# Kernel tuning notes

Measured on AMD Instinct MI355X. Metric: run time of the kernel, lower is better.

The kernel has to match this reference:

```python
import jax, jax.numpy as jnp
import numpy as np

NUM_ENTITIES = 100000
NUM_TIMES = 10000
D = 512
DB = 768
NUM_REL = 200
NUM_BASES = 4
N_NODES = 30000
N_EDGES = 200000
B = 128
P_ENT = 64
P_TIME = 32
T_UNIQ = 2000


def setup_inputs() -> dict:
    key = jax.random.key(0)
    ks = jax.random.split(key, 32)
    n = jax.random.normal
    ri = jax.random.randint
    inp = {}
    # learned params
    inp['emb'] = n(ks[0], (NUM_ENTITIES + NUM_TIMES, D), jnp.float32) * 0.05
    sc = 1.0 / np.sqrt(D)
    inp['basis1'] = n(ks[1], (NUM_BASES, D, D), jnp.float32) * sc
    inp['att1'] = n(ks[2], (NUM_REL, NUM_BASES), jnp.float32) * 0.5
    inp['root1'] = n(ks[3], (D, D), jnp.float32) * sc
    inp['bias1'] = jnp.zeros((D,), jnp.float32)
    inp['basis2'] = n(ks[4], (NUM_BASES, D, D), jnp.float32) * sc
    inp['att2'] = n(ks[5], (NUM_REL, NUM_BASES), jnp.float32) * 0.5
    inp['root2'] = n(ks[6], (D, D), jnp.float32) * sc
    inp['bias2'] = jnp.zeros((D,), jnp.float32)
    sb = 1.0 / np.sqrt(DB)
    inp['W_lin'] = n(ks[7], (DB, D), jnp.float32) * sb
    inp['b_lin'] = jnp.zeros((D,), jnp.float32)
    inp['W_attn'] = n(ks[8], (DB, D), jnp.float32) * sb
    inp['b_attn'] = jnp.zeros((D,), jnp.float32)
    inp['W_prob'] = n(ks[9], (DB, 1), jnp.float32) * sb
    inp['b_prob'] = jnp.zeros((1,), jnp.float32)
    # forward tensor args
    inp['ques_emb_bert'] = n(ks[10], (B, DB), jnp.float32)
    inp['x_idx'] = ri(ks[11], (N_NODES,), 0, NUM_ENTITIES, jnp.int32)
    inp['edge_index'] = ri(ks[12], (2, N_EDGES), 0, N_NODES, jnp.int32)
    inp['edge_type'] = ri(ks[13], (N_EDGES,), 0, NUM_REL, jnp.int32)
    inp['start_time'] = ri(ks[14], (N_EDGES,), 0, NUM_TIMES, jnp.int32)
    inp['end_time'] = ri(ks[15], (N_EDGES,), 0, NUM_TIMES, jnp.int32)
    inp['edge_batch_idx'] = jnp.sort(ri(ks[16], (N_EDGES,), 0, B, jnp.int32))
    inp['edge_norm'] = jax.random.uniform(ks[17], (N_EDGES,), jnp.float32)
    inp['uniq_times'] = ri(ks[18], (T_UNIQ,), 0, NUM_TIMES, jnp.int32)
    # padded index vectors: positions >= count point at the appended zero row
    ent_counts = ri(ks[19], (B,), 1, P_ENT + 1, jnp.int32)
    time_counts = ri(ks[20], (B,), 1, P_TIME + 1, jnp.int32)
    pe = ri(ks[21], (B, P_ENT), 0, N_NODES, jnp.int32)
    pt = ri(ks[22], (B, P_TIME), 0, T_UNIQ, jnp.int32)
    inp['padded_ent'] = jnp.where(jnp.arange(P_ENT)[None, :] < ent_counts[:, None], pe, N_NODES)
    inp['padded_time'] = jnp.where(jnp.arange(P_TIME)[None, :] < time_counts[:, None], pt, T_UNIQ)
    inp['ent_counts'] = ent_counts
    inp['time_counts'] = time_counts
    return inp


def rgcn_layer(x, basis, att, root, bias, src, dst, etype, st_emb, et_emb, q_t, edge_norm):
    # basis decomposition: project all nodes through each basis once. [N, NB, D]
    xb = jnp.einsum('ni,bio->nbo', x, basis)
    coeff = att[etype]                                 # [E, NB]
    msg = jnp.einsum('eb,ebd->ed', coeff, xb[src])     # [E, D]
    # time gate: question-time embedding vs edge interval midpoint embedding
    gate = jax.nn.sigmoid(jnp.sum(q_t * 0.5 * (st_emb + et_emb), axis=-1))  # [E]
    msg = msg * (gate * edge_norm)[:, None]
    agg = jax.ops.segment_sum(msg, dst, num_segments=N_NODES)
    return agg + x @ root + bias


def reference(emb, basis1, att1, root1, bias1, basis2, att2, root2, bias2,
              W_lin, b_lin, W_attn, b_attn, W_prob, b_prob,
              ques_emb_bert, x_idx, edge_index, edge_type, start_time, end_time,
              edge_batch_idx, edge_norm, uniq_times, padded_ent, padded_time,
              ent_counts, time_counts):
    question_embedding = ques_emb_bert @ W_lin + b_lin                  # [B, D]
    time_for_edge_attn = (ques_emb_bert @ W_attn + b_attn)[edge_batch_idx]  # [E, D]
    st_emb = emb[start_time + NUM_ENTITIES]
    et_emb = emb[end_time + NUM_ENTITIES]
    x = emb[x_idx]                                                      # [N, D]
    src, dst = edge_index[0], edge_index[1]
    h = jax.nn.relu(rgcn_layer(x, basis1, att1, root1, bias1, src, dst, edge_type,
                               st_emb, et_emb, time_for_edge_attn, edge_norm))
    # dropout is identity in eval mode
    h = rgcn_layer(h, basis2, att2, root2, bias2, src, dst, edge_type,
                   st_emb, et_emb, time_for_edge_attn, edge_norm)       # [N, D]
    subgraph_time_emb = emb[uniq_times + NUM_ENTITIES]                  # [T_u, D]
    zero = jnp.zeros((1, D), h.dtype)
    ent_w_zeros = jnp.concatenate([h, zero], axis=0)
    time_w_zeros = jnp.concatenate([subgraph_time_emb, zero], axis=0)
    pooled_ent = jnp.sum(ent_w_zeros[padded_ent], axis=1) / ent_counts[:, None].astype(h.dtype)
    pooled_time = jnp.sum(time_w_zeros[padded_time], axis=1) / time_counts[:, None].astype(h.dtype)
    p_ent = jax.nn.sigmoid(ques_emb_bert @ W_prob + b_prob)             # [B, 1]
    pred = (question_embedding + pooled_ent * p_ent + pooled_time * (1.0 - p_ent)) / 3.0
    # batched cosine similarity against full entity+time vocab
    pred_n = pred / jnp.maximum(jnp.linalg.norm(pred, axis=-1, keepdims=True), 1e-8)
    emb_n = emb / jnp.maximum(jnp.linalg.norm(emb, axis=-1, keepdims=True), 1e-8)
    score = pred_n @ emb_n.T                                            # [B, V]
    return score * 30.0
```

## Files before the change

kernel.cpp:

```cpp
#include <hip/hip_runtime.h>

#define NUM_ENT   100000
#define NTIMES    10000
#define DD        512
#define DB        768
#define NREL      200
#define NBAS      4
#define NN        30000
#define NEDGE     200000
#define BATCH     128
#define PENT      64
#define PTIME     32
#define TUNIQ     2000
#define V_TOT     110000
#define V_PAD     110208
#define VT16      6888
#define M_PAD2    30208
#define MT2R      1888
#define KT_L      80
#define KT_E      16

typedef __attribute__((ext_vector_type(8))) short s8v;
typedef __attribute__((ext_vector_type(4))) float f4v;

__device__ __forceinline__ unsigned short f2bf(float x){
  unsigned int u = __builtin_bit_cast(unsigned int, x);
  u += 0x7fffu + ((u >> 16) & 1u);
  return (unsigned short)(u >> 16);
}
__device__ __forceinline__ float bf2f(unsigned short h){
  unsigned int u = ((unsigned int)h) << 16;
  return __builtin_bit_cast(float, u);
}

__device__ __forceinline__ void gload16(const void* g, void* l){
  __builtin_amdgcn_global_load_lds(
      (const __attribute__((address_space(1))) void*)g,
      (__attribute__((address_space(3))) void*)l, 16, 0, 0);
}


__global__ __launch_bounds__(256) void k_conv_emb(const float* __restrict__ emb,
    unsigned short* __restrict__ Bp, float* __restrict__ invn){
  int vt = blockIdx.x;
  int wid = threadIdx.x >> 6, lane = threadIdx.x & 63;
  int vrow = vt * 16 + (lane & 15);
  float ss = 0.f;
  __shared__ float ssw[4][16];
  for (int i = 0; i < 4; ++i){
    int kt = wid + i * 4;
    int k0 = kt * 32 + (lane >> 4) * 8;
    s8v o;
    if (vrow < V_TOT){
      const float4* p = reinterpret_cast<const float4*>(emb + (size_t)vrow * DD + k0);
      float4 v0 = p[0], v1 = p[1];
      ss += v0.x*v0.x + v0.y*v0.y + v0.z*v0.z + v0.w*v0.w;
      ss += v1.x*v1.x + v1.y*v1.y + v1.z*v1.z + v1.w*v1.w;
      o[0] = (short)f2bf(v0.x); o[1] = (short)f2bf(v0.y);
      o[2] = (short)f2bf(v0.z); o[3] = (short)f2bf(v0.w);
      o[4] = (short)f2bf(v1.x); o[5] = (short)f2bf(v1.y);
      o[6] = (short)f2bf(v1.z); o[7] = (short)f2bf(v1.w);
    } else {
      #pragma unroll
      for (int j = 0; j < 8; ++j) o[j] = 0;
    }
    *reinterpret_cast<s8v*>(Bp + ((size_t)(kt * VT16 + vt) << 9) + lane * 8) = o;
  }
  ss += __shfl_xor(ss, 16);
  ss += __shfl_xor(ss, 32);
  if ((lane >> 4) == 0) ssw[wid][lane] = ss;
  __syncthreads();
  if (threadIdx.x < 16){
    float s = ssw[0][threadIdx.x] + ssw[1][threadIdx.x] + ssw[2][threadIdx.x] + ssw[3][threadIdx.x];
    int v = vt * 16 + threadIdx.x;
    invn[v] = (v < V_TOT) ? (1.0f / fmaxf(sqrtf(s), 1e-8f)) : 0.0f;
  }
}

__global__ __launch_bounds__(256) void k_small2(const float* __restrict__ ques,
    const float* __restrict__ Wl, const float* __restrict__ bl,
    const float* __restrict__ Wa, const float* __restrict__ ba,
    const float* __restrict__ Wp, const float* __restrict__ bp,
    float* __restrict__ qlin, float* __restrict__ qattn, float* __restrict__ pent){
  if (blockIdx.x == 32){
    int b = threadIdx.x >> 1, half = threadIdx.x & 1;
    float a = 0.f;
    int k0 = half * 384;
    for (int k = k0; k < k0 + 384; ++k)
      a = fmaf(ques[(size_t)b * DB + k], Wp[k], a);
    a += __shfl_xor(a, 1);
    if (half == 0) pent[b] = 1.f / (1.f + expf(-(a + bp[0])));
    return;
  }
  __shared__ float sq[128 * 96];
  int col = threadIdx.x & 31, bg = threadIdx.x >> 5;
  int c0 = blockIdx.x * 32;
  const float* W = (c0 < 512) ? Wl : Wa;
  int wcol = (c0 & 511) + col;
  float acc[16] = {};
  for (int k0 = 0; k0 < DB; k0 += 96){
    __syncthreads();
    for (int i = threadIdx.x; i < 128 * 96; i += 256){
      int b = i / 96, kk = i - b * 96;
      sq[i] = ques[(size_t)b * DB + k0 + kk];
    }
    __syncthreads();
    for (int kk = 0; kk < 96; kk += 4){
      float w0 = W[(size_t)(k0 + kk + 0) * 512 + wcol];
      float w1 = W[(size_t)(k0 + kk + 1) * 512 + wcol];
      float w2 = W[(size_t)(k0 + kk + 2) * 512 + wcol];
      float w3 = W[(size_t)(k0 + kk + 3) * 512 + wcol];
      #pragma unroll
      for (int bb = 0; bb < 16; ++bb){
        float4 qv = *reinterpret_cast<const float4*>(&sq[(bg * 16 + bb) * 96 + kk]);
        acc[bb] = fmaf(qv.x, w0, fmaf(qv.y, w1, fmaf(qv.z, w2, fmaf(qv.w, w3, acc[bb]))));
      }
    }
  }
  float* dst = (c0 < 512) ? qlin : qattn;
  const float* bias = (c0 < 512) ? bl : ba;
  #pragma unroll
  for (int bb = 0; bb < 16; ++bb)
    dst[(size_t)(bg * 16 + bb) * 512 + wcol] = acc[bb] + bias[wcol];
}

__global__ __launch_bounds__(256) void k_pack_qrows(const float* __restrict__ src,
    unsigned short* __restrict__ Ap){
  int w = (int)((blockIdx.x * 256 + threadIdx.x) >> 6);
  int lane = threadIdx.x & 63;
  if (w >= BATCH) return;
  const float* p = src + (size_t)w * 512 + lane * 8;
  s8v o;
  #pragma unroll
  for (int j = 0; j < 8; ++j) o[j] = (short)f2bf(p[j]);
  *reinterpret_cast<s8v*>(Ap + ((size_t)((w >> 4) * KT_E + (lane >> 2)) << 9)
                             + ((w & 15) + (lane & 3) * 16) * 8) = o;
}

__global__ __launch_bounds__(256) void k_pack_B2(
    const float* __restrict__ basis1, const float* __restrict__ root1,
    const float* __restrict__ basis2, const float* __restrict__ root2,
    unsigned short* __restrict__ B1p, unsigned short* __restrict__ B2p){
  int idx = blockIdx.x * 256 + threadIdx.x;
  int set = idx >= KT_L * 32 * 64;
  if (set) idx -= KT_L * 32 * 64;
  const float* basis = set ? basis2 : basis1;
  const float* root  = set ? root2  : root1;
  unsigned short* Bp = set ? B2p : B1p;
  int lane = idx & 63; int kt = idx >> 11;
  int k0 = kt * 32 + (lane >> 4) * 8;
  int col = ((idx >> 6) & 31) * 16 + (lane & 15);
  s8v o;
  #pragma unroll
  for (int j = 0; j < 8; ++j){
    int k = k0 + j;
    float v = (k < 2048) ? basis[(size_t)k * 512 + col] : root[(size_t)(k - 2048) * 512 + col];
    o[j] = (short)f2bf(v);
  }
  *reinterpret_cast<s8v*>(Bp + (size_t)idx * 8) = o;
}

__global__ __launch_bounds__(256) void k_gemm_m2(
    const unsigned short* __restrict__ A, const unsigned short* __restrict__ B,
    float* __restrict__ outf){
  __shared__ __align__(1024) short sAll[3 * 8192];
  const int Kt = KT_E;
  int tid = threadIdx.x;
  int lane = tid & 63, wid = tid >> 6;
  int wr = wid >> 1, wc = wid & 1;
  int rt0 = blockIdx.x * 8;
  int ct0 = blockIdx.y * 8;
  const unsigned short* pA0 = A + ((size_t)(rt0 + 2 * wid) * Kt) * 512 + lane * 8;
  const unsigned short* pA1 = pA0 + (size_t)Kt * 512;
  const unsigned short* pB0 = B + (size_t)(ct0 + 2 * wid) * 512 + lane * 8;
  const unsigned short* pB1 = pB0 + 512;
  size_t gbs = (size_t)VT16 * 512;
  int so = 2 * wid * 512;
  f4v acc[4][4] = {};

  auto STAGE = [&](int buf, int kt){
    short* b = &sAll[buf * 8192];
    gload16(pA0 + (size_t)kt * 512, b + so);
    gload16(pA1 + (size_t)kt * 512, b + so + 512);
    gload16(pB0 + (size_t)kt * gbs, b + 4096 + so);
    gload16(pB1 + (size_t)kt * gbs, b + 4096 + so + 512);
  };
  auto COMPUTE = [&](int buf){
    const short* base = &sAll[buf * 8192];
    s8v af[4], bfr[4];
    #pragma unroll
    for (int m = 0; m < 4; ++m) af[m] = *reinterpret_cast<const s8v*>(base + (wr * 4 + m) * 512 + lane * 8);
    #pragma unroll
    for (int n = 0; n < 4; ++n) bfr[n] = *reinterpret_cast<const s8v*>(base + 4096 + (wc * 4 + n) * 512 + lane * 8);
    #pragma unroll
    for (int m = 0; m < 4; ++m)
      #pragma unroll
      for (int n = 0; n < 4; ++n)
        acc[m][n] = __builtin_amdgcn_mfma_f32_16x16x32_bf16(af[m], bfr[n], acc[m][n], 0, 0, 0);
  };

  STAGE(0, 0);
  STAGE(1, 1);
  int cb = 0, sb = 2;
  for (int kt = 0; kt < Kt - 2; ++kt){
    STAGE(sb, kt + 2);
    asm volatile("s_waitcnt vmcnt(8)" ::: "memory");
    __builtin_amdgcn_s_barrier();
    __builtin_amdgcn_sched_barrier(0);
    COMPUTE(cb);
    __builtin_amdgcn_s_barrier();
    cb = (cb == 2) ? 0 : cb + 1;
    sb = (sb == 2) ? 0 : sb + 1;
  }
  asm volatile("s_waitcnt vmcnt(4)" ::: "memory");
  __builtin_amdgcn_s_barrier();
  __builtin_amdgcn_sched_barrier(0);
  COMPUTE(cb);
  cb = (cb == 2) ? 0 : cb + 1;
  asm volatile("s_waitcnt vmcnt(0)" ::: "memory");
  __builtin_amdgcn_s_barrier();
  __builtin_amdgcn_sched_barrier(0);
  COMPUTE(cb);

  #pragma unroll
  for (int m = 0; m < 4; ++m)
    #pragma unroll
    for (int n = 0; n < 4; ++n){
      int row0 = rt0 * 16 + (wr * 4 + m) * 16 + ((lane >> 4) * 4);
      int col  = (ct0 + wc * 4 + n) * 16 + (lane & 15);
      #pragma unroll
      for (int r = 0; r < 4; ++r){
        int rr = row0 + r;
        if (col < NTIMES) outf[(size_t)rr * NTIMES + col] = acc[m][n][r];
      }
    }
}

__global__ __launch_bounds__(256, 3) void k_score_p(
    const unsigned short* __restrict__ Apred, const unsigned short* __restrict__ Bp,
    const float* __restrict__ invn, float* __restrict__ out){
  __shared__ __align__(1024) short sAll[3 * 8192];
  const int Kt = KT_E;
  int tid = threadIdx.x;
  int lane = tid & 63, wid = tid >> 6;
  int wr = wid >> 1, wc = wid & 1;
  int kq = lane >> 4, r16 = lane & 15;
  int ct0 = blockIdx.x * 8;
  const unsigned short* pA0 = Apred + ((size_t)(2 * wid) * Kt) * 512 + lane * 8;
  const unsigned short* pA1 = pA0 + (size_t)Kt * 512;
  const unsigned short* pB0 = Bp + (size_t)(ct0 + 2 * wid) * 512 + lane * 8;
  const unsigned short* pB1 = pB0 + 512;
  size_t gbs = (size_t)VT16 * 512;
  int so = 2 * wid * 512;
  f4v acc[4][4] = {};

  auto STAGE = [&](int buf, int kt){
    short* b = &sAll[buf * 8192];
    gload16(pA0 + (size_t)kt * 512, b + so);
    gload16(pA1 + (size_t)kt * 512, b + so + 512);
    gload16(pB0 + (size_t)kt * gbs, b + 4096 + so);
    gload16(pB1 + (size_t)kt * gbs, b + 4096 + so + 512);
  };
  auto COMPUTE = [&](int buf){
    const short* base = &sAll[buf * 8192];
    s8v af[4], bfr[4];
    #pragma unroll
    for (int m = 0; m < 4; ++m) af[m] = *reinterpret_cast<const s8v*>(base + (wr * 4 + m) * 512 + lane * 8);
    #pragma unroll
    for (int n = 0; n < 4; ++n) bfr[n] = *reinterpret_cast<const s8v*>(base + 4096 + (wc * 4 + n) * 512 + lane * 8);
    #pragma unroll
    for (int m = 0; m < 4; ++m)
      #pragma unroll
      for (int n = 0; n < 4; ++n)
        acc[m][n] = __builtin_amdgcn_mfma_f32_16x16x32_bf16(af[m], bfr[n], acc[m][n], 0, 0, 0);
  };

  STAGE(0, 0);
  STAGE(1, 1);
  int cb = 0, sb = 2;
  for (int kt = 0; kt < Kt - 2; ++kt){
    STAGE(sb, kt + 2);
    asm volatile("s_waitcnt vmcnt(8)" ::: "memory");
    __builtin_amdgcn_s_barrier();
    __builtin_amdgcn_sched_barrier(0);
    COMPUTE(cb);
    __builtin_amdgcn_s_barrier();
    cb = (cb == 2) ? 0 : cb + 1;
    sb = (sb == 2) ? 0 : sb + 1;
  }
  asm volatile("s_waitcnt vmcnt(4)" ::: "memory");
  __builtin_amdgcn_s_barrier();
  __builtin_amdgcn_sched_barrier(0);
  COMPUTE(cb);
  cb = (cb == 2) ? 0 : cb + 1;
  asm volatile("s_waitcnt vmcnt(0)" ::: "memory");
  __builtin_amdgcn_s_barrier();
  __builtin_amdgcn_sched_barrier(0);
  COMPUTE(cb);

  __syncthreads();
  float* scratch = reinterpret_cast<float*>(sAll) + wid * 2176;
  int colg = ct0 * 16 + wc * 64 + r16 * 4;
  bool c_ok = colg < V_TOT;
  float4 inv4 = float4{0.f, 0.f, 0.f, 0.f};
  if (c_ok){
    inv4 = *reinterpret_cast<const float4*>(invn + colg);
    inv4.x *= 30.f; inv4.y *= 30.f; inv4.z *= 30.f; inv4.w *= 30.f;
  }
  #pragma unroll
  for (int p = 0; p < 2; ++p){
    #pragma unroll
    for (int mm = 0; mm < 2; ++mm){
      int m = p * 2 + mm;
      #pragma unroll
      for (int n = 0; n < 4; ++n)
        #pragma unroll
        for (int r = 0; r < 4; ++r)
          scratch[(mm * 16 + kq * 4 + r) * 68 + n * 16 + r16] = acc[m][n][r];
    }
    #pragma unroll
    for (int i = 0; i < 8; ++i){
      int row_r = i * 4 + kq;
      float4 v = *reinterpret_cast<const float4*>(scratch + row_r * 68 + r16 * 4);
      if (c_ok){
        float4 o;
        o.x = v.x * inv4.x; o.y = v.y * inv4.y; o.z = v.z * inv4.z; o.w = v.w * inv4.w;
        int grr = wr * 64 + p * 32 + row_r;
        *reinterpret_cast<float4*>(out + (size_t)grr * V_TOT + colg) = o;
      }
    }
  }
}

template<int MODE>
__global__ __launch_bounds__(512, 2) void k_gemm512(
    const unsigned short* __restrict__ A, const unsigned short* __restrict__ B,
    const float* __restrict__ bias, unsigned short* __restrict__ outh){
  __shared__ __align__(1024) short sAll[3 * 20480];
  const int Kt = KT_L;
  int tid = threadIdx.x;
  int lane = tid & 63, wid = tid >> 6;
  int wr = wid >> 2, wc = wid & 3;
  int blk = blockIdx.x;
  int rt0 = blk * 8;
  const unsigned short* pA = A + ((size_t)(rt0 + wid) * Kt) * 512 + lane * 8;
  const unsigned short* pB = B + (size_t)(wid * 4) * 512 + lane * 8;
  int soA = wid * 512;
  int soB = 4096 + wid * 4 * 512;
  f4v acc[4][8] = {};

  auto STAGE = [&](int buf, int kt){
    short* b = &sAll[buf * 20480];
    gload16(pA + (size_t)kt * 512, b + soA);
    const unsigned short* pb = pB + (size_t)kt * 32 * 512;
    gload16(pb,        b + soB);
    gload16(pb +  512, b + soB +  512);
    gload16(pb + 1024, b + soB + 1024);
    gload16(pb + 1536, b + soB + 1536);
  };
  auto COMPUTE = [&](int buf){
    const short* base = &sAll[buf * 20480];
    s8v af[4], bfr[8];
    #pragma unroll
    for (int m = 0; m < 4; ++m) af[m] = *reinterpret_cast<const s8v*>(base + (wr * 4 + m) * 512 + lane * 8);
    #pragma unroll
    for (int n = 0; n < 8; ++n) bfr[n] = *reinterpret_cast<const s8v*>(base + 4096 + (wc * 8 + n) * 512 + lane * 8);
    __builtin_amdgcn_s_setprio(1);
    #pragma unroll
    for (int m = 0; m < 4; ++m)
      #pragma unroll
      for (int n = 0; n < 8; ++n)
        acc[m][n] = __builtin_amdgcn_mfma_f32_16x16x32_bf16(af[m], bfr[n], acc[m][n], 0, 0, 0);
    __builtin_amdgcn_s_setprio(0);
  };

  STAGE(0, 0);
  STAGE(1, 1);
  int cb = 0, sb = 2;
  for (int kt = 0; kt < Kt - 2; ++kt){
    STAGE(sb, kt + 2);
    asm volatile("s_waitcnt vmcnt(10)" ::: "memory");
    __builtin_amdgcn_s_barrier();
    __builtin_amdgcn_sched_barrier(0);
    COMPUTE(cb);
    __builtin_amdgcn_s_barrier();
    cb = (cb == 2) ? 0 : cb + 1;
    sb = (sb == 2) ? 0 : sb + 1;
  }
  asm volatile("s_waitcnt vmcnt(5)" ::: "memory");
  __builtin_amdgcn_s_barrier();
  __builtin_amdgcn_sched_barrier(0);
  COMPUTE(cb);
  cb = (cb == 2) ? 0 : cb + 1;
  asm volatile("s_waitcnt vmcnt(0)" ::: "memory");
  __builtin_amdgcn_s_barrier();
  __builtin_amdgcn_sched_barrier(0);
  COMPUTE(cb);

  int R0 = blk * 128 + wr * 64 + ((lane >> 4) * 4);
  int C0 = wc * 128 + (lane & 15);
  #pragma unroll
  for (int m = 0; m < 4; ++m)
    #pragma unroll
    for (int r4 = 0; r4 < 4; ++r4){
      int rr = R0 + m * 16 + r4;
      if (rr < NN){
        #pragma unroll
        for (int n = 0; n < 8; ++n){
          int col = C0 + n * 16;
          float v = acc[m][n][r4] + bias[col];
          if constexpr (MODE == 1) v = fmaxf(v, 0.f);
          outh[(size_t)rr * 512 + col] = f2bf(v);
        }
      }
    }
}

__global__ __launch_bounds__(256) void k_edgeprep(const int* __restrict__ ebatch,
    const int* __restrict__ st, const int* __restrict__ et,
    const float* __restrict__ enorm, const float* __restrict__ M2,
    const int* __restrict__ ei,
    float* __restrict__ we, int* __restrict__ cnt, int* __restrict__ lists){
  int e = blockIdx.x * 256 + threadIdx.x;
  if (e >= NEDGE) return;
  int b = ebatch[e];
  float s = 0.5f * (M2[(size_t)b * NTIMES + st[e]] + M2[(size_t)b * NTIMES + et[e]]);
  we[e] = (1.f / (1.f + expf(-s))) * enorm[e];
  int dst = ei[NEDGE + e];
  int slot = atomicAdd(&cnt[dst], 1);
  if (slot < 64) lists[(size_t)dst * 64 + slot] = e;
}

__global__ __launch_bounds__(256) void k_gather_x(const int* __restrict__ x_idx,
    const float* __restrict__ emb, unsigned short* __restrict__ Ap,
    unsigned short* __restrict__ x_rm){
  int w = (int)((blockIdx.x * 256 + threadIdx.x) >> 6);
  int lane = threadIdx.x & 63;
  if (w >= NN) return;
  int v = x_idx[w];
  const float4* p = reinterpret_cast<const float4*>(emb + (size_t)v * 512 + lane * 8);
  float4 a = p[0], b = p[1];
  s8v x;
  x[0] = (short)f2bf(a.x); x[1] = (short)f2bf(a.y); x[2] = (short)f2bf(a.z); x[3] = (short)f2bf(a.w);
  x[4] = (short)f2bf(b.x); x[5] = (short)f2bf(b.y); x[6] = (short)f2bf(b.z); x[7] = (short)f2bf(b.w);
  *reinterpret_cast<s8v*>(x_rm + (size_t)w * 512 + lane * 8) = x;
  *reinterpret_cast<s8v*>(Ap + ((size_t)(w >> 4) * KT_L + 64 + (lane >> 2)) * 512
                             + ((w & 15) + (lane & 3) * 16) * 8) = x;
}

__global__ __launch_bounds__(256) void k_pack_rows(const unsigned short* __restrict__ src_rm,
    unsigned short* __restrict__ Ap){
  int w = (int)((blockIdx.x * 256 + threadIdx.x) >> 6);
  int lane = threadIdx.x & 63;
  if (w >= NN) return;
  s8v x = *reinterpret_cast<const s8v*>(src_rm + (size_t)w * 512 + lane * 8);
  *reinterpret_cast<s8v*>(Ap + ((size_t)(w >> 4) * KT_L + 64 + (lane >> 2)) * 512
                             + ((w & 15) + (lane & 3) * 16) * 8) = x;
}

__global__ __launch_bounds__(256) void k_edge_agg(const unsigned short* __restrict__ xsrc,
    const int* __restrict__ ei, const int* __restrict__ etype,
    const float* __restrict__ we, const float* __restrict__ att,
    const int* __restrict__ cnt, const int* __restrict__ lists,
    unsigned short* __restrict__ Ap){
  __shared__ float satt[NREL * NBAS];
  __shared__ int sed[4][64];
  for (int i = threadIdx.x; i < NREL * NBAS; i += 256) satt[i] = att[i];
  int wid = threadIdx.x >> 6, lane = threadIdx.x & 63;
  int n = blockIdx.x * 4 + wid;
  int deg = min(cnt[n], 64);
  int eid = (lane < deg) ? lists[(size_t)n * 64 + lane] : 0x7fffffff;
  int rank = 0;
  for (int j = 0; j < 64; ++j){
    int v = __shfl(eid, j);
    rank += (v < eid) ? 1 : 0;
  }
  __syncthreads();
  if (lane < deg) sed[wid][rank] = eid;
  __syncthreads();
  float acc[NBAS][8] = {};
  if (deg > 0){
    int my_e = sed[wid][(lane < deg) ? lane : 0];
    int my_s = ei[my_e];
    int my_t = etype[my_e];
    float my_w = we[my_e];
    float c0l = my_w * satt[my_t * 4 + 0];
    float c1l = my_w * satt[my_t * 4 + 1];
    float c2l = my_w * satt[my_t * 4 + 2];
    float c3l = my_w * satt[my_t * 4 + 3];
    int s0 = __shfl(my_s, 0);
    s8v xv = *reinterpret_cast<const s8v*>(xsrc + (size_t)s0 * 512 + lane * 8);
    for (int j = 0; j < deg; ++j){
      s8v xn = xv;
      if (j + 1 < deg){
        int sn = __shfl(my_s, j + 1);
        xn = *reinterpret_cast<const s8v*>(xsrc + (size_t)sn * 512 + lane * 8);
      }
      float c0 = __shfl(c0l, j), c1 = __shfl(c1l, j);
      float c2 = __shfl(c2l, j), c3 = __shfl(c3l, j);
      #pragma unroll
      for (int jj = 0; jj < 8; ++jj){
        float x = bf2f((unsigned short)xv[jj]);
        acc[0][jj] = fmaf(c0, x, acc[0][jj]);
        acc[1][jj] = fmaf(c1, x, acc[1][jj]);
        acc[2][jj] = fmaf(c2, x, acc[2][jj]);
        acc[3][jj] = fmaf(c3, x, acc[3][jj]);
      }
      xv = xn;
    }
  }
  #pragma unroll
  for (int b = 0; b < NBAS; ++b){
    s8v o;
    #pragma unroll
    for (int jj = 0; jj < 8; ++jj) o[jj] = (short)f2bf(acc[b][jj]);
    *reinterpret_cast<s8v*>(Ap + ((size_t)(n >> 4) * KT_L + b * 16 + (lane >> 2)) * 512
                               + ((n & 15) + (lane & 3) * 16) * 8) = o;
  }
}

__global__ __launch_bounds__(256) void k_pred(const unsigned short* __restrict__ h2,
    const float* __restrict__ emb, const int* __restrict__ uniq,
    const int* __restrict__ pent_idx, const int* __restrict__ ptime_idx,
    const int* __restrict__ ent_c, const int* __restrict__ time_c,
    const float* __restrict__ qlin, const float* __restrict__ pent,
    unsigned short* __restrict__ Ap_pred){
  __shared__ float sacc[4][512];
  int b = blockIdx.x;
  int wid = threadIdx.x >> 6, lane = threadIdx.x & 63;
  float a[8] = {};
  if (wid < 2){
    for (int j = wid * 32; j < wid * 32 + 32; ++j){
      int idx = pent_idx[b * PENT + j];
      if (idx < NN){
        s8v hv = *reinterpret_cast<const s8v*>(h2 + (size_t)idx * 512 + lane * 8);
        #pragma unroll
        for (int jj = 0; jj < 8; ++jj) a[jj] += bf2f((unsigned short)hv[jj]);
      }
    }
  } else {
    for (int j = (wid - 2) * 16; j < (wid - 2) * 16 + 16; ++j){
      int ti = ptime_idx[b * PTIME + j];
      if (ti < TUNIQ){
        const float* p = emb + (size_t)(NUM_ENT + uniq[ti]) * 512 + lane * 8;
        #pragma unroll
        for (int jj = 0; jj < 8; ++jj) a[jj] += p[jj];
      }
    }
  }
  #pragma unroll
  for (int jj = 0; jj < 8; ++jj) sacc[wid][lane * 8 + jj] = a[jj];
  __syncthreads();
  if (wid == 0){
    float ce = 1.f / (float)ent_c[b], ct = 1.f / (float)time_c[b];
    float p = pent[b];
    float pr[8]; float ss = 0.f;
    #pragma unroll
    for (int jj = 0; jj < 8; ++jj){
      int i = lane * 8 + jj;
      float ae = sacc[0][i] + sacc[1][i];
      float at = sacc[2][i] + sacc[3][i];
      float v = (qlin[(size_t)b * 512 + i] + ae * ce * p + at * ct * (1.f - p)) * (1.f / 3.f);
      pr[jj] = v; ss += v * v;
    }
    ss += __shfl_xor(ss, 32); ss += __shfl_xor(ss, 16); ss += __shfl_xor(ss, 8);
    ss += __shfl_xor(ss, 4);  ss += __shfl_xor(ss, 2);  ss += __shfl_xor(ss, 1);
    float inv = 1.f / fmaxf(sqrtf(ss), 1e-8f);
    s8v o;
    #pragma unroll
    for (int jj = 0; jj < 8; ++jj) o[jj] = (short)f2bf(pr[jj] * inv);
    *reinterpret_cast<s8v*>(Ap_pred + ((size_t)((b >> 4) * KT_E + (lane >> 2)) << 9)
                                    + ((b & 15) + (lane & 3) * 16) * 8) = o;
  }
}

extern "C" void kernel_launch(void* const* d_in, const int* in_sizes, int n_in,
                              void* d_out, int out_size, void* d_ws, size_t ws_size,
                              hipStream_t stream){
  const float* emb    = (const float*)d_in[0];
  const float* basis1 = (const float*)d_in[1];
  const float* att1   = (const float*)d_in[2];
  const float* root1  = (const float*)d_in[3];
  const float* bias1  = (const float*)d_in[4];
  const float* basis2 = (const float*)d_in[5];
  const float* att2   = (const float*)d_in[6];
  const float* root2  = (const float*)d_in[7];
  const float* bias2  = (const float*)d_in[8];
  const float* W_lin  = (const float*)d_in[9];
  const float* b_lin  = (const float*)d_in[10];
  const float* W_attn = (const float*)d_in[11];
  const float* b_attn = (const float*)d_in[12];
  const float* W_prob = (const float*)d_in[13];
  const float* b_prob = (const float*)d_in[14];
  const float* ques   = (const float*)d_in[15];
  const int* x_idx    = (const int*)d_in[16];
  const int* eidx     = (const int*)d_in[17];
  const int* etype    = (const int*)d_in[18];
  const int* stime    = (const int*)d_in[19];
  const int* etime    = (const int*)d_in[20];
  const int* ebatch   = (const int*)d_in[21];
  const float* enorm  = (const float*)d_in[22];
  const int* uniq     = (const int*)d_in[23];
  const int* pent_i   = (const int*)d_in[24];
  const int* ptime_i  = (const int*)d_in[25];
  const int* ent_c    = (const int*)d_in[26];
  const int* time_c   = (const int*)d_in[27];
  float* out = (float*)d_out;

  char* w = (char*)d_ws;
  size_t off = 0;
  auto alloc = [&](size_t bytes)->char*{ char* p = w + off; off += (bytes + 255) & ~(size_t)255; return p; };
  unsigned short* Bp_emb = (unsigned short*)alloc((size_t)KT_E * VT16 * 1024);
  float*          invn   = (float*)alloc((size_t)V_PAD * 4);
  unsigned short* Ap   = (unsigned short*)alloc((size_t)MT2R * KT_L * 1024);
  unsigned short* B1p  = (unsigned short*)alloc((size_t)KT_L * 32 * 1024);
  unsigned short* B2p  = (unsigned short*)alloc((size_t)KT_L * 32 * 1024);
  char* xh_base = alloc((size_t)NN * 512 * 2 * 2);
  unsigned short* x_rm = (unsigned short*)xh_base;
  unsigned short* h1   = (unsigned short*)(xh_base + (size_t)NN * 512 * 2);
  unsigned short* h2   = (unsigned short*)xh_base;
  float* M2    = (float*)alloc((size_t)BATCH * NTIMES * 4);
  float* we    = (float*)alloc((size_t)NEDGE * 4);
  float* qlin  = (float*)alloc((size_t)BATCH * 512 * 4);
  float* qattn = (float*)alloc((size_t)BATCH * 512 * 4);
  float* pent  = (float*)alloc(1024);
  unsigned short* Apq    = (unsigned short*)alloc((size_t)8 * KT_E * 1024);
  unsigned short* Appred = (unsigned short*)alloc((size_t)8 * KT_E * 1024);
  int* cnt   = (int*)alloc((size_t)NN * 4);
  int* lists = (int*)alloc((size_t)NN * 64 * 4);
  (void)ws_size; (void)in_sizes; (void)n_in; (void)out_size;

  k_small2<<<33, 256, 0, stream>>>(ques, W_lin, b_lin, W_attn, b_attn, W_prob, b_prob,
                                   qlin, qattn, pent);
  k_pack_qrows<<<32, 256, 0, stream>>>(qattn, Apq);
  k_conv_emb<<<VT16, 256, 0, stream>>>(emb, Bp_emb, invn);
  k_pack_B2<<<2 * (KT_L * 32 * 64) / 256, 256, 0, stream>>>(basis1, root1, basis2, root2,
                                                            B1p, B2p);
  k_gemm_m2<<<dim3(1, 79), 256, 0, stream>>>(Apq, Bp_emb + (size_t)6250 * 512, M2);
  hipMemsetAsync(cnt, 0, (size_t)NN * 4, stream);
  k_edgeprep<<<(NEDGE + 255) / 256, 256, 0, stream>>>(ebatch, stime, etime, enorm, M2,
                                                      eidx, we, cnt, lists);
  k_gather_x<<<NN / 4, 256, 0, stream>>>(x_idx, emb, Ap, x_rm);
  k_edge_agg<<<NN / 4, 256, 0, stream>>>(x_rm, eidx, etype, we, att1, cnt, lists, Ap);
  k_gemm512<1><<<236, 512, 0, stream>>>(Ap, B1p, bias1, h1);
  k_pack_rows<<<NN / 4, 256, 0, stream>>>(h1, Ap);
  k_edge_agg<<<NN / 4, 256, 0, stream>>>(h1, eidx, etype, we, att2, cnt, lists, Ap);
  k_gemm512<2><<<236, 512, 0, stream>>>(Ap, B2p, bias2, h2);
  k_pred<<<BATCH, 256, 0, stream>>>(h2, emb, uniq, pent_i, ptime_i, ent_c, time_c,
                                    qlin, pent, Appred);
  k_score_p<<<861, 256, 0, stream>>>(Appred, Bp_emb, invn, out);
}
```

Measured before the change: 691.7 us.

## Merge prep kernels and fuse row packing into GEMM and projection epilogues

Three setup kernels (embedding conversion, weight packing, node gather) are combined into one launch that branches on block index. The qattn bf16 packing now happens directly in the k_small2 epilogue, and the first-layer GEMM writes its output straight into the packed A tail, so the separate pack kernels go away. This cuts kernel launches and an intermediate round trip through global memory. In exchange, the GEMM and projection epilogues now issue scattered 2-byte stores into the packed layout.

```diff
diff --git a/kernel.cpp b/kernel.cpp
--- a/kernel.cpp
+++ b/kernel.cpp
@@ -19,6 +19,8 @@
 #define MT2R      1888
 #define KT_L      80
 #define KT_E      16
+#define PACKB_BLKS 1280
+#define GATH_BLKS  7500
 
 typedef __attribute__((ext_vector_type(8))) short s8v;
 typedef __attribute__((ext_vector_type(4))) float f4v;
@@ -40,40 +42,80 @@
 }
 
 
-__global__ __launch_bounds__(256) void k_conv_emb(const float* __restrict__ emb,
-    unsigned short* __restrict__ Bp, float* __restrict__ invn){
-  int vt = blockIdx.x;
-  int wid = threadIdx.x >> 6, lane = threadIdx.x & 63;
-  int vrow = vt * 16 + (lane & 15);
-  float ss = 0.f;
-  __shared__ float ssw[4][16];
-  for (int i = 0; i < 4; ++i){
-    int kt = wid + i * 4;
+__global__ __launch_bounds__(256) void k_prep(const float* __restrict__ emb,
+    const float* __restrict__ basis1, const float* __restrict__ root1,
+    const float* __restrict__ basis2, const float* __restrict__ root2,
+    const int* __restrict__ x_idx,
+    unsigned short* __restrict__ Bp, float* __restrict__ invn,
+    unsigned short* __restrict__ B1p, unsigned short* __restrict__ B2p,
+    unsigned short* __restrict__ Ap, unsigned short* __restrict__ x_rm){
+  int bid = blockIdx.x;
+  if (bid < VT16){
+    int vt = bid;
+    int wid = threadIdx.x >> 6, lane = threadIdx.x & 63;
+    int vrow = vt * 16 + (lane & 15);
+    float ss = 0.f;
+    __shared__ float ssw[4][16];
+    for (int i = 0; i < 4; ++i){
+      int kt = wid + i * 4;
+      int k0 = kt * 32 + (lane >> 4) * 8;
+      s8v o;
+      if (vrow < V_TOT){
+        const float4* p = reinterpret_cast<const float4*>(emb + (size_t)vrow * DD + k0);
+        float4 v0 = p[0], v1 = p[1];
+        ss += v0.x*v0.x + v0.y*v0.y + v0.z*v0.z + v0.w*v0.w;
+        ss += v1.x*v1.x + v1.y*v1.y + v1.z*v1.z + v1.w*v1.w;
+        o[0] = (short)f2bf(v0.x); o[1] = (short)f2bf(v0.y);
+        o[2] = (short)f2bf(v0.z); o[3] = (short)f2bf(v0.w);
+        o[4] = (short)f2bf(v1.x); o[5] = (short)f2bf(v1.y);
+        o[6] = (short)f2bf(v1.z); o[7] = (short)f2bf(v1.w);
+      } else {
+        #pragma unroll
+        for (int j = 0; j < 8; ++j) o[j] = 0;
+      }
+      *reinterpret_cast<s8v*>(Bp + ((size_t)(kt * VT16 + vt) << 9) + lane * 8) = o;
+    }
+    ss += __shfl_xor(ss, 16);
+    ss += __shfl_xor(ss, 32);
+    if ((lane >> 4) == 0) ssw[wid][lane] = ss;
+    __syncthreads();
+    if (threadIdx.x < 16){
+      float s = ssw[0][threadIdx.x] + ssw[1][threadIdx.x] + ssw[2][threadIdx.x] + ssw[3][threadIdx.x];
+      int v = vt * 16 + threadIdx.x;
+      invn[v] = (v < V_TOT) ? (1.0f / fmaxf(sqrtf(s), 1e-8f)) : 0.0f;
+    }
+  } else if (bid < VT16 + PACKB_BLKS){
+    int idx = (bid - VT16) * 256 + threadIdx.x;
+    int set = idx >= KT_L * 32 * 64;
+    if (set) idx -= KT_L * 32 * 64;
+    const float* basis = set ? basis2 : basis1;
+    const float* root  = set ? root2  : root1;
+    unsigned short* Bw = set ? B2p : B1p;
+    int lane = idx & 63; int kt = idx >> 11;
     int k0 = kt * 32 + (lane >> 4) * 8;
+    int col = ((idx >> 6) & 31) * 16 + (lane & 15);
     s8v o;
-    if (vrow < V_TOT){
-      const float4* p = reinterpret_cast<const float4*>(emb + (size_t)vrow * DD + k0);
-      float4 v0 = p[0], v1 = p[1];
-      ss += v0.x*v0.x + v0.y*v0.y + v0.z*v0.z + v0.w*v0.w;
-      ss += v1.x*v1.x + v1.y*v1.y + v1.z*v1.z + v1.w*v1.w;
-      o[0] = (short)f2bf(v0.x); o[1] = (short)f2bf(v0.y);
-      o[2] = (short)f2bf(v0.z); o[3] = (short)f2bf(v0.w);
-      o[4] = (short)f2bf(v1.x); o[5] = (short)f2bf(v1.y);
-      o[6] = (short)f2bf(v1.z); o[7] = (short)f2bf(v1.w);
-    } else {
-      #pragma unroll
-      for (int j = 0; j < 8; ++j) o[j] = 0;
-    }
-    *reinterpret_cast<s8v*>(Bp + ((size_t)(kt * VT16 + vt) << 9) + lane * 8) = o;
-  }
-  ss += __shfl_xor(ss, 16);
-  ss += __shfl_xor(ss, 32);
-  if ((lane >> 4) == 0) ssw[wid][lane] = ss;
-  __syncthreads();
-  if (threadIdx.x < 16){
-    float s = ssw[0][threadIdx.x] + ssw[1][threadIdx.x] + ssw[2][threadIdx.x] + ssw[3][threadIdx.x];
-    int v = vt * 16 + threadIdx.x;
-    invn[v] = (v < V_TOT) ? (1.0f / fmaxf(sqrtf(s), 1e-8f)) : 0.0f;
+    #pragma unroll
+    for (int j = 0; j < 8; ++j){
+      int k = k0 + j;
+      float v = (k < 2048) ? basis[(size_t)k * 512 + col] : root[(size_t)(k - 2048) * 512 + col];
+      o[j] = (short)f2bf(v);
+    }
+    *reinterpret_cast<s8v*>(Bw + (size_t)idx * 8) = o;
+  } else {
+    int gb = bid - (VT16 + PACKB_BLKS);
+    int w = (int)((gb * 256 + threadIdx.x) >> 6);
+    int lane = threadIdx.x & 63;
+    if (w >= NN) return;
+    int v = x_idx[w];
+    const float4* p = reinterpret_cast<const float4*>(emb + (size_t)v * 512 + lane * 8);
+    float4 a = p[0], b = p[1];
+    s8v x;
+    x[0] = (short)f2bf(a.x); x[1] = (short)f2bf(a.y); x[2] = (short)f2bf(a.z); x[3] = (short)f2bf(a.w);
+    x[4] = (short)f2bf(b.x); x[5] = (short)f2bf(b.y); x[6] = (short)f2bf(b.z); x[7] = (short)f2bf(b.w);
+    *reinterpret_cast<s8v*>(x_rm + (size_t)w * 512 + lane * 8) = x;
+    *reinterpret_cast<s8v*>(Ap + ((size_t)(w >> 4) * KT_L + 64 + (lane >> 2)) * 512
+                               + ((w & 15) + (lane & 3) * 16) * 8) = x;
   }
 }
 
@@ -81,7 +123,8 @@
     const float* __restrict__ Wl, const float* __restrict__ bl,
     const float* __restrict__ Wa, const float* __restrict__ ba,
     const float* __restrict__ Wp, const float* __restrict__ bp,
-    float* __restrict__ qlin, float* __restrict__ qattn, float* __restrict__ pent){
+    float* __restrict__ qlin, unsigned short* __restrict__ Apq,
+    float* __restrict__ pent){
   if (blockIdx.x == 32){
     int b = threadIdx.x >> 1, half = threadIdx.x & 1;
     float a = 0.f;
@@ -117,47 +160,20 @@
       }
     }
   }
-  float* dst = (c0 < 512) ? qlin : qattn;
-  const float* bias = (c0 < 512) ? bl : ba;
-  #pragma unroll
-  for (int bb = 0; bb < 16; ++bb)
-    dst[(size_t)(bg * 16 + bb) * 512 + wcol] = acc[bb] + bias[wcol];
-}
-
-__global__ __launch_bounds__(256) void k_pack_qrows(const float* __restrict__ src,
-    unsigned short* __restrict__ Ap){
-  int w = (int)((blockIdx.x * 256 + threadIdx.x) >> 6);
-  int lane = threadIdx.x & 63;
-  if (w >= BATCH) return;
-  const float* p = src + (size_t)w * 512 + lane * 8;
-  s8v o;
-  #pragma unroll
-  for (int j = 0; j < 8; ++j) o[j] = (short)f2bf(p[j]);
-  *reinterpret_cast<s8v*>(Ap + ((size_t)((w >> 4) * KT_E + (lane >> 2)) << 9)
-                             + ((w & 15) + (lane & 3) * 16) * 8) = o;
-}
-
-__global__ __launch_bounds__(256) void k_pack_B2(
-    const float* __restrict__ basis1, const float* __restrict__ root1,
-    const float* __restrict__ basis2, const float* __restrict__ root2,
-    unsigned short* __restrict__ B1p, unsigned short* __restrict__ B2p){
-  int idx = blockIdx.x * 256 + threadIdx.x;
-  int set = idx >= KT_L * 32 * 64;
-  if (set) idx -= KT_L * 32 * 64;
-  const float* basis = set ? basis2 : basis1;
-  const float* root  = set ? root2  : root1;
-  unsigned short* Bp = set ? B2p : B1p;
-  int lane = idx & 63; int kt = idx >> 11;
-  int k0 = kt * 32 + (lane >> 4) * 8;
-  int col = ((idx >> 6) & 31) * 16 + (lane & 15);
-  s8v o;
-  #pragma unroll
-  for (int j = 0; j < 8; ++j){
-    int k = k0 + j;
-    float v = (k < 2048) ? basis[(size_t)k * 512 + col] : root[(size_t)(k - 2048) * 512 + col];
-    o[j] = (short)f2bf(v);
-  }
-  *reinterpret_cast<s8v*>(Bp + (size_t)idx * 8) = o;
+  if (c0 < 512){
+    #pragma unroll
+    for (int bb = 0; bb < 16; ++bb)
+      qlin[(size_t)(bg * 16 + bb) * 512 + wcol] = acc[bb] + bl[wcol];
+  } else {
+    float bb_ = ba[wcol];
+    size_t base = ((size_t)bg * 16 + (wcol >> 5)) * 512
+                + ((wcol >> 3) & 3) * 128 + (wcol & 7);
+    #pragma unroll
+    for (int bb = 0; bb < 16; ++bb){
+      int w = bg * 16 + bb;
+      Apq[base + (w & 15) * 8] = f2bf(acc[bb] + bb_);
+    }
+  }
 }
 
 __global__ __launch_bounds__(256) void k_gemm_m2(
@@ -335,7 +351,8 @@
 template<int MODE>
 __global__ __launch_bounds__(512, 2) void k_gemm512(
     const unsigned short* __restrict__ A, const unsigned short* __restrict__ B,
-    const float* __restrict__ bias, unsigned short* __restrict__ outh){
+    const float* __restrict__ bias, unsigned short* __restrict__ outh,
+    unsigned short* __restrict__ Ap_tail){
   __shared__ __align__(1024) short sAll[3 * 20480];
   const int Kt = KT_L;
   int tid = threadIdx.x;
@@ -409,8 +426,15 @@
         for (int n = 0; n < 8; ++n){
           int col = C0 + n * 16;
           float v = acc[m][n][r4] + bias[col];
-          if constexpr (MODE == 1) v = fmaxf(v, 0.f);
-          outh[(size_t)rr * 512 + col] = f2bf(v);
+          if constexpr (MODE == 1){
+            v = fmaxf(v, 0.f);
+            unsigned short hv = f2bf(v);
+            outh[(size_t)rr * 512 + col] = hv;
+            Ap_tail[((size_t)(rr >> 4) * KT_L + 64 + (col >> 5)) * 512
+                    + ((rr & 15) + ((col >> 3) & 3) * 16) * 8 + (col & 7)] = hv;
+          } else {
+            outh[(size_t)rr * 512 + col] = f2bf(v);
+          }
         }
       }
     }
@@ -429,33 +453,6 @@
   int dst = ei[NEDGE + e];
   int slot = atomicAdd(&cnt[dst], 1);
   if (slot < 64) lists[(size_t)dst * 64 + slot] = e;
-}
-
-__global__ __launch_bounds__(256) void k_gather_x(const int* __restrict__ x_idx,
-    const float* __restrict__ emb, unsigned short* __restrict__ Ap,
-    unsigned short* __restrict__ x_rm){
-  int w = (int)((blockIdx.x * 256 + threadIdx.x) >> 6);
-  int lane = threadIdx.x & 63;
-  if (w >= NN) return;
-  int v = x_idx[w];
-  const float4* p = reinterpret_cast<const float4*>(emb + (size_t)v * 512 + lane * 8);
-  float4 a = p[0], b = p[1];
-  s8v x;
-  x[0] = (short)f2bf(a.x); x[1] = (short)f2bf(a.y); x[2] = (short)f2bf(a.z); x[3] = (short)f2bf(a.w);
-  x[4] = (short)f2bf(b.x); x[5] = (short)f2bf(b.y); x[6] = (short)f2bf(b.z); x[7] = (short)f2bf(b.w);
-  *reinterpret_cast<s8v*>(x_rm + (size_t)w * 512 + lane * 8) = x;
-  *reinterpret_cast<s8v*>(Ap + ((size_t)(w >> 4) * KT_L + 64 + (lane >> 2)) * 512
-                             + ((w & 15) + (lane & 3) * 16) * 8) = x;
-}
-
-__global__ __launch_bounds__(256) void k_pack_rows(const unsigned short* __restrict__ src_rm,
-    unsigned short* __restrict__ Ap){
-  int w = (int)((blockIdx.x * 256 + threadIdx.x) >> 6);
-  int lane = threadIdx.x & 63;
-  if (w >= NN) return;
-  s8v x = *reinterpret_cast<const s8v*>(src_rm + (size_t)w * 512 + lane * 8);
-  *reinterpret_cast<s8v*>(Ap + ((size_t)(w >> 4) * KT_L + 64 + (lane >> 2)) * 512
-                             + ((w & 15) + (lane & 3) * 16) * 8) = x;
 }
 
 __global__ __launch_bounds__(256) void k_edge_agg(const unsigned short* __restrict__ xsrc,
@@ -622,7 +619,6 @@
   float* M2    = (float*)alloc((size_t)BATCH * NTIMES * 4);
   float* we    = (float*)alloc((size_t)NEDGE * 4);
   float* qlin  = (float*)alloc((size_t)BATCH * 512 * 4);
-  float* qattn = (float*)alloc((size_t)BATCH * 512 * 4);
   float* pent  = (float*)alloc(1024);
   unsigned short* Apq    = (unsigned short*)alloc((size_t)8 * KT_E * 1024);
   unsigned short* Appred = (unsigned short*)alloc((size_t)8 * KT_E * 1024);
@@ -630,22 +626,19 @@
   int* lists = (int*)alloc((size_t)NN * 64 * 4);
   (void)ws_size; (void)in_sizes; (void)n_in; (void)out_size;
 
+  k_prep<<<VT16 + PACKB_BLKS + GATH_BLKS, 256, 0, stream>>>(
+      emb, basis1, root1, basis2, root2, x_idx,
+      Bp_emb, invn, B1p, B2p, Ap, x_rm);
   k_small2<<<33, 256, 0, stream>>>(ques, W_lin, b_lin, W_attn, b_attn, W_prob, b_prob,
-                                   qlin, qattn, pent);
-  k_pack_qrows<<<32, 256, 0, stream>>>(qattn, Apq);
-  k_conv_emb<<<VT16, 256, 0, stream>>>(emb, Bp_emb, invn);
-  k_pack_B2<<<2 * (KT_L * 32 * 64) / 256, 256, 0, stream>>>(basis1, root1, basis2, root2,
-                                                            B1p, B2p);
+                                   qlin, Apq, pent);
   k_gemm_m2<<<dim3(1, 79), 256, 0, stream>>>(Apq, Bp_emb + (size_t)6250 * 512, M2);
   hipMemsetAsync(cnt, 0, (size_t)NN * 4, stream);
   k_edgeprep<<<(NEDGE + 255) / 256, 256, 0, stream>>>(ebatch, stime, etime, enorm, M2,
                                                       eidx, we, cnt, lists);
-  k_gather_x<<<NN / 4, 256, 0, stream>>>(x_idx, emb, Ap, x_rm);
   k_edge_agg<<<NN / 4, 256, 0, stream>>>(x_rm, eidx, etype, we, att1, cnt, lists, Ap);
-  k_gemm512<1><<<236, 512, 0, stream>>>(Ap, B1p, bias1, h1);
-  k_pack_rows<<<NN / 4, 256, 0, stream>>>(h1, Ap);
+  k_gemm512<1><<<236, 512, 0, stream>>>(Ap, B1p, bias1, h1, Ap);
   k_edge_agg<<<NN / 4, 256, 0, stream>>>(h1, eidx, etype, we, att2, cnt, lists, Ap);
-  k_gemm512<2><<<236, 512, 0, stream>>>(Ap, B2p, bias2, h2);
+  k_gemm512<2><<<236, 512, 0, stream>>>(Ap, B2p, bias2, h2, nullptr);
   k_pred<<<BATCH, 256, 0, stream>>>(h2, emb, uniq, pent_i, ptime_i, ent_c, time_c,
                                     qlin, pent, Appred);
   k_score_p<<<861, 256, 0, stream>>>(Appred, Bp_emb, invn, out);
```

After: 676.9 us. 1.02x faster.
